# Performance work log

Hardware: AMD Instinct MI355X
Metric: run time of the kernel (lower is better)

Reference implementation:

```python
import jax, jax.numpy as jnp
import numpy as np


def _gru(x, Wih, Whh, bih, bhh):
    """Single-layer torch-style GRU, batch_first. x:[B,T,E], Wih:[3H,E], Whh:[3H,H]."""
    gi = jnp.einsum('bte,ge->btg', x, Wih) + bih  # precompute input gates [B,T,3H]
    H = Whh.shape[1]
    h0 = jnp.zeros((x.shape[0], H), x.dtype)

    def step(h, gi_t):
        gh = h @ Whh.T + bhh
        i_r, i_z, i_n = jnp.split(gi_t, 3, axis=-1)
        h_r, h_z, h_n = jnp.split(gh, 3, axis=-1)
        r = jax.nn.sigmoid(i_r + h_r)
        z = jax.nn.sigmoid(i_z + h_z)
        n = jnp.tanh(i_n + r * h_n)
        h_new = (1.0 - z) * n + z * h
        return h_new, h_new

    _, hs = jax.lax.scan(step, h0, jnp.swapaxes(gi, 0, 1))
    return jnp.swapaxes(hs, 0, 1)  # [B,T,H]


def setup_inputs() -> dict:
    V, E, H, B, S, Tc, Ts = 100000, 256, 256, 256, 10, 20, 50
    Bc = B * S
    k = jax.random.split(jax.random.key(0), 16)
    w = lambda kk, shp, s=0.05: (jax.random.normal(kk, shp) * s).astype(jnp.float32)
    return {
        'input_cate_batch': jax.random.randint(k[0], (Bc, Tc), 0, V),
        'mask_cate_batch': jnp.ones((Bc, Tc), jnp.float32),
        'mask_cate_seq_batch': jnp.ones((B, S), jnp.float32),
        'max_actionNum_cate_batch': Tc,
        'max_subseqNum_cate_batch': S,
        'subseqLen_cate_batch': jax.random.randint(k[1], (Bc,), 0, Tc),
        'seqLen_cate_batch': jax.random.randint(k[2], (B,), 0, S),
        'input_batch': jax.random.randint(k[3], (B, Ts), 0, V),
        'mask_batch': jnp.ones((B, Ts), jnp.float32),
        'seqLen_batch': jax.random.randint(k[4], (B,), 0, Ts),
        'target_y_batch': jax.random.randint(k[5], (B,), 0, V),
        'train_test_flag': 0,
        'emb': w(k[6], (V, E), 0.02),
        'Wih_c': w(k[7], (3 * H, E)), 'Whh_c': w(k[8], (3 * H, H)),
        'bih_c': jnp.zeros((3 * H,), jnp.float32), 'bhh_c': jnp.zeros((3 * H,), jnp.float32),
        'Wih_s': w(k[9], (3 * H, E)), 'Whh_s': w(k[10], (3 * H, H)),
        'bih_s': jnp.zeros((3 * H,), jnp.float32), 'bhh_s': jnp.zeros((3 * H,), jnp.float32),
        'fc_W': w(k[11], (H, 2 * H)), 'fc_b': jnp.zeros((H,), jnp.float32),
    }


def reference(input_cate_batch, mask_cate_batch, mask_cate_seq_batch,
              max_actionNum_cate_batch, max_subseqNum_cate_batch,
              subseqLen_cate_batch, seqLen_cate_batch, input_batch, mask_batch,
              seqLen_batch, target_y_batch, train_test_flag,
              emb, Wih_c, Whh_c, bih_c, bhh_c, Wih_s, Whh_s, bih_s, bhh_s,
              fc_W, fc_b):
    Bc = input_cate_batch.shape[0]
    B = input_batch.shape[0]
    S = max_subseqNum_cate_batch
    # --- category GRU over subsequences ---
    x_c = emb[input_cate_batch]                                  # [Bc,Tc,E]
    out_c = _gru(x_c, Wih_c, Whh_c, bih_c, bhh_c) * mask_cate_batch[:, :, None]
    gathered = out_c[jnp.arange(Bc), subseqLen_cate_batch]       # [Bc,H] per-row length gather
    seq_cate = gathered.reshape(B, S, -1)                        # [B,S,H]
    # --- short GRU over the recent session ---
    x_s = emb[input_batch]                                       # [B,Ts,E]
    out_s = _gru(x_s, Wih_s, Whh_s, bih_s, bhh_s) * mask_batch[:, :, None]
    out_short = out_s[jnp.arange(B), seqLen_batch]               # [B,H]
    # --- masked softmax attention of short state over subseq states ---
    att = jnp.einsum('bsh,bh->bs', seq_cate, out_short)          # [B,S]
    w = jax.nn.softmax(att, axis=1) * mask_cate_seq_batch
    w = w / jnp.sum(w, axis=1, keepdims=True)
    sum_cate = jnp.einsum('bs,bsh->bh', w, seq_cate)             # [B,H]
    mix = jnp.concatenate([sum_cate, out_short], axis=1)         # [B,2H]
    fc_out = mix @ fc_W.T + fc_b                                 # [B,H]
    logits = fc_out @ emb.T                                      # [B,V] shared-embedding output layer
    return logits, target_y_batch
```

## Files before the change

### kernel.cpp

```cpp
#include <hip/hip_runtime.h>
#include <cmath>

#define EMB_V 100000
#define BATCH 256
#define SUBS  10
#define BC    2560
#define TC    20
#define TS    50

using bf16x8 = __attribute__((ext_vector_type(8))) short;
using f32x4  = __attribute__((ext_vector_type(4))) float;

__device__ __forceinline__ unsigned short f2bf(float f) {
    unsigned int u = __float_as_uint(f);
    u += 0x7fff + ((u >> 16) & 1);
    return (unsigned short)(u >> 16);
}
__device__ __forceinline__ float bf2f(unsigned short u) {
    return __uint_as_float(((unsigned int)u) << 16);
}
__device__ __forceinline__ float bf_lo(unsigned u) { return __uint_as_float(u << 16); }
__device__ __forceinline__ float bf_hi(unsigned u) { return __uint_as_float(u & 0xffff0000u); }
__device__ __forceinline__ float sigmoid_fast(float x) {
    return __builtin_amdgcn_rcpf(1.f + __expf(-x));
}
__device__ __forceinline__ float tanh_fast(float x) {
    float e = __expf(2.f * x);
    return 1.f - 2.f * __builtin_amdgcn_rcpf(e + 1.f);
}
__device__ __forceinline__ void dma16(const void* g, void* l) {
    __builtin_amdgcn_global_load_lds((const __attribute__((address_space(1))) void*)g,
                                     (__attribute__((address_space(3))) void*)l, 16, 0, 0);
}

__device__ __forceinline__ void pack_whh_dev(const float* __restrict__ W,
                                             unsigned short* __restrict__ P, int t) {
    if (t >= 48 * 8 * 64) return;
    int l = t & 63, kc = (t >> 6) & 7, nt = t >> 9;
    int g = nt % 3, cg = nt / 3;
    int n = g * 256 + (cg >> 1) * 32 + 2 * (l & 15) + (cg & 1);
    int k = kc * 32 + (l >> 4) * 8;
    const float* src = W + n * 256 + k;
    unsigned short* dst = P + (size_t)t * 8;
#pragma unroll
    for (int j = 0; j < 8; ++j) dst[j] = f2bf(src[j]);
}
__global__ __launch_bounds__(256) void prep_misc(
    const float* __restrict__ fc_W, float* __restrict__ fcWT,
    const float* __restrict__ Whh_c, unsigned short* __restrict__ packW_c,
    const float* __restrict__ Whh_s, unsigned short* __restrict__ packW_s,
    const float* __restrict__ Wih_c, unsigned short* __restrict__ wihb_c,
    const float* __restrict__ Wih_s, unsigned short* __restrict__ wihb_s)
{
    const int b = blockIdx.x, tid = threadIdx.x;
    if (b < 512) {
        int o = b * 256 + tid;
        int c = o >> 8, r = o & 255;
        fcWT[o] = fc_W[r * 512 + c];
    } else if (b < 608) {
        pack_whh_dev(Whh_c, packW_c, (b - 512) * 256 + tid);
    } else if (b < 704) {
        pack_whh_dev(Whh_s, packW_s, (b - 608) * 256 + tid);
    } else if (b < 896) {
        int i = (b - 704) * 256 + tid;
        float4 v = ((const float4*)Wih_c)[i];
        ((ushort4*)wihb_c)[i] = make_ushort4(f2bf(v.x), f2bf(v.y), f2bf(v.z), f2bf(v.w));
    } else {
        int i = (b - 896) * 256 + tid;
        float4 v = ((const float4*)Wih_s)[i];
        ((ushort4*)wihb_s)[i] = make_ushort4(f2bf(v.x), f2bf(v.y), f2bf(v.z), f2bf(v.w));
    }
}

__global__ void f32_to_bf16(const float* __restrict__ in, unsigned short* __restrict__ out,
                            int n4) {
    for (int i = blockIdx.x * 256 + threadIdx.x; i < n4; i += gridDim.x * 256) {
        float4 v = ((const float4*)in)[i];
        ((ushort4*)out)[i] = make_ushort4(f2bf(v.x), f2bf(v.y), f2bf(v.z), f2bf(v.w));
    }
}

template <bool GATHER, bool OBF16, bool NGUARD>
__global__ __launch_bounds__(256, 3) void gemm_abt(
    const unsigned short* __restrict__ A, const int* __restrict__ tok,
    const unsigned short* __restrict__ B, void* __restrict__ Cout,
    int N, int ldc)
{
    __shared__ unsigned short Asub[128 * 64];
    __shared__ unsigned short Bsub[128 * 64];
    const int tid = threadIdx.x;
    const int l = tid & 63, wave = tid >> 6;
    const int lm = l & 15, quad = l >> 4;
    const int wm = wave >> 1, wn = wave & 1;
    const int n0 = blockIdx.x * 128, m0 = blockIdx.y * 128;

    unsigned aofs[4], bofs[4];
#pragma unroll
    for (int i = 0; i < 4; ++i) {
        int c = tid + i * 256, row = c >> 3, cc = c & 7;
        int sw = cc ^ (row & 7);
        aofs[i] = (GATHER ? (unsigned)tok[m0 + row] : (unsigned)(m0 + row)) * 256u + sw * 8u;
        unsigned brow = (unsigned)(n0 + row);
        if (NGUARD && brow >= (unsigned)N) brow = (unsigned)N - 1;
        bofs[i] = brow * 256u + sw * 8u;
    }
    const int dstu = (tid & 192) * 8;
    const int fsw = lm & 7;

    f32x4 acc[4][4];
#pragma unroll
    for (int mi = 0; mi < 4; ++mi)
#pragma unroll
        for (int ni = 0; ni < 4; ++ni) acc[mi][ni] = (f32x4){0.f, 0.f, 0.f, 0.f};

    for (int kk = 0; kk < 4; ++kk) {
        const int k0 = kk * 64;
#pragma unroll
        for (int i = 0; i < 4; ++i)
            dma16(A + aofs[i] + k0, &Asub[dstu + i * 2048]);
#pragma unroll
        for (int i = 0; i < 4; ++i)
            dma16(B + bofs[i] + k0, &Bsub[dstu + i * 2048]);
        __syncthreads();
#pragma unroll
        for (int kc = 0; kc < 2; ++kc) {
            const int ch = ((kc * 4 + quad) ^ fsw) * 8;
            bf16x8 af[4], bfv[4];
#pragma unroll
            for (int mi = 0; mi < 4; ++mi)
                af[mi] = *(const bf16x8*)&Asub[(wm * 64 + mi * 16 + lm) * 64 + ch];
#pragma unroll
            for (int ni = 0; ni < 4; ++ni)
                bfv[ni] = *(const bf16x8*)&Bsub[(wn * 64 + ni * 16 + lm) * 64 + ch];
#pragma unroll
            for (int mi = 0; mi < 4; ++mi)
#pragma unroll
                for (int ni = 0; ni < 4; ++ni)
                    acc[mi][ni] = __builtin_amdgcn_mfma_f32_16x16x32_bf16(
                        af[mi], bfv[ni], acc[mi][ni], 0, 0, 0);
        }
        __syncthreads();
    }
#pragma unroll
    for (int mi = 0; mi < 4; ++mi)
#pragma unroll
        for (int ni = 0; ni < 4; ++ni) {
            int col = n0 + wn * 64 + ni * 16 + lm;
            if (NGUARD && col >= N) continue;
#pragma unroll
            for (int i = 0; i < 4; ++i) {
                int row = m0 + wm * 64 + mi * 16 + quad * 4 + i;
                if (OBF16)
                    ((unsigned short*)Cout)[(size_t)row * ldc + col] = f2bf(acc[mi][ni][i]);
                else
                    ((float*)Cout)[(size_t)row * ldc + col] = acc[mi][ni][i];
            }
        }
}

__global__ __launch_bounds__(512, 1) void gru_scan_fused(
    const unsigned short* __restrict__ gi_c, const unsigned short* __restrict__ pW_c,
    const float* __restrict__ bih_c, const float* __restrict__ bhh_c,
    const int* __restrict__ len_c, const float* __restrict__ mask_c,
    float* __restrict__ out_c,
    const unsigned short* __restrict__ gi_s, const unsigned short* __restrict__ pW_s,
    const float* __restrict__ bih_s, const float* __restrict__ bhh_s,
    const int* __restrict__ len_s, const float* __restrict__ mask_s,
    float* __restrict__ out_s)
{
    __shared__ unsigned short h_lds[2][16][264];
    __shared__ unsigned short b_lds[8 * 8 * 512];

    const bool is_cat = blockIdx.x < (BC / 16);
    const int  T      = is_cat ? TC : TS;
    const int  R      = is_cat ? blockIdx.x : blockIdx.x - BC / 16;
    const int  row0   = R * 16;
    const unsigned short* gi   = is_cat ? gi_c  : gi_s;
    const unsigned short* pW   = is_cat ? pW_c  : pW_s;
    const float*          bih  = is_cat ? bih_c : bih_s;
    const float*          bhh  = is_cat ? bhh_c : bhh_s;
    const int*            lenp = is_cat ? len_c : len_s;
    const float*          mask = is_cat ? mask_c : mask_s;
    float*                outp = is_cat ? out_c : out_s;

    const int tid  = threadIdx.x;
    const int l    = tid & 63, w = tid >> 6;
    const int lm   = l & 15,   quad = l >> 4;

    for (int i = tid; i < 2 * 16 * 264; i += 512) ((unsigned short*)h_lds)[i] = 0;

    bf16x8 breg[40];
#pragma unroll
    for (int ti = 0; ti < 6; ++ti)
#pragma unroll
        for (int kc = 0; kc < 8; ++kc) {
            bf16x8 v = *((const bf16x8*)pW + (size_t)((6 * w + ti) * 8 + kc) * 64 + l);
            if (ti < 5) breg[ti * 8 + kc] = v;
            else        *(bf16x8*)&b_lds[((w * 8 + kc) * 64 + l) * 8] = v;
        }

    const int c0p = 32 * w + 2 * lm;
    const float cR0 = bih[c0p] + bhh[c0p],             cR1 = bih[c0p + 1] + bhh[c0p + 1];
    const float cZ0 = bih[256 + c0p] + bhh[256 + c0p], cZ1 = bih[257 + c0p] + bhh[257 + c0p];
    const float cNi0 = bih[512 + c0p], cNi1 = bih[513 + c0p];
    const float cNh0 = bhh[512 + c0p], cNh1 = bhh[513 + c0p];

    int len[4];
    const unsigned short* gpa[4];
#pragma unroll
    for (int i = 0; i < 4; ++i) {
        const int r = quad * 4 + i;
        len[i] = lenp[row0 + r];
        gpa[i] = gi + (size_t)(row0 + r) * T * 768 + c0p;
    }

    float hold0[4] = {0.f, 0.f, 0.f, 0.f};
    float hold1[4] = {0.f, 0.f, 0.f, 0.f};

    __syncthreads();

    for (int t = 0; t < T; ++t) {
        unsigned gv[4][3];
#pragma unroll
        for (int i = 0; i < 4; ++i) {
            const unsigned short* p = gpa[i];
            gv[i][0] = *(const unsigned*)(p);
            gv[i][1] = *(const unsigned*)(p + 256);
            gv[i][2] = *(const unsigned*)(p + 512);
            gpa[i] = p + 768;
        }

        const unsigned short (*hb)[264] = h_lds[t & 1];
        f32x4 acc[6];
#pragma unroll
        for (int ti = 0; ti < 6; ++ti) acc[ti] = (f32x4){0.f, 0.f, 0.f, 0.f};
#pragma unroll
        for (int kc = 0; kc < 8; ++kc) {
            bf16x8 a = *(const bf16x8*)&hb[lm][kc * 32 + quad * 8];
#pragma unroll
            for (int ti = 0; ti < 6; ++ti) {
                bf16x8 b = (ti < 5) ? breg[ti * 8 + kc]
                                    : *(const bf16x8*)&b_lds[((w * 8 + kc) * 64 + l) * 8];
                acc[ti] = __builtin_amdgcn_mfma_f32_16x16x32_bf16(a, b, acc[ti], 0, 0, 0);
            }
        }

        unsigned short (*hw)[264] = h_lds[(t + 1) & 1];
#pragma unroll
        for (int i = 0; i < 4; ++i) {
            const int r = quad * 4 + i;
            float rg0 = sigmoid_fast(bf_lo(gv[i][0]) + acc[0][i] + cR0);
            float rg1 = sigmoid_fast(bf_hi(gv[i][0]) + acc[3][i] + cR1);
            float zg0 = sigmoid_fast(bf_lo(gv[i][1]) + acc[1][i] + cZ0);
            float zg1 = sigmoid_fast(bf_hi(gv[i][1]) + acc[4][i] + cZ1);
            float ng0 = tanh_fast(bf_lo(gv[i][2]) + cNi0 + rg0 * (acc[2][i] + cNh0));
            float ng1 = tanh_fast(bf_hi(gv[i][2]) + cNi1 + rg1 * (acc[5][i] + cNh1));
            float hn0 = zg0 * (hold0[i] - ng0) + ng0;
            float hn1 = zg1 * (hold1[i] - ng1) + ng1;
            hold0[i] = hn0; hold1[i] = hn1;
            *(unsigned*)&hw[r][c0p] = (unsigned)f2bf(hn0) | ((unsigned)f2bf(hn1) << 16);
            if (t == len[i]) {
                float m = mask[(row0 + r) * T + t];
                *(float2*)&outp[(size_t)(row0 + r) * 256 + c0p] = make_float2(hn0 * m, hn1 * m);
            }
        }

        asm volatile("s_waitcnt lgkmcnt(0)" ::: "memory");
        __builtin_amdgcn_sched_barrier(0);
        __builtin_amdgcn_s_barrier();
        __builtin_amdgcn_sched_barrier(0);
    }
}

__global__ __launch_bounds__(256) void attn_fc(
    const float* __restrict__ seq_cate, const float* __restrict__ out_short,
    const float* __restrict__ mask_seq, const float* __restrict__ fcWT,
    const float* __restrict__ fc_b, const int* __restrict__ target,
    unsigned short* __restrict__ fc_out, float* __restrict__ d_out)
{
    __shared__ float sc[SUBS][256];
    __shared__ float os[256];
    __shared__ float part[SUBS][256];
    __shared__ float mix[512];
    const int b = blockIdx.x, tid = threadIdx.x;

    os[tid] = out_short[b * 256 + tid];
    for (int s = 0; s < SUBS; ++s) sc[s][tid] = seq_cate[(size_t)(b * SUBS + s) * 256 + tid];
    __syncthreads();

    for (int s = 0; s < SUBS; ++s) part[s][tid] = sc[s][tid] * os[tid];
    __syncthreads();
    for (int off = 128; off >= 1; off >>= 1) {
        if (tid < off)
            for (int s = 0; s < SUBS; ++s) part[s][tid] += part[s][tid + off];
        __syncthreads();
    }

    float w[SUBS];
    float m = -1e30f;
    for (int s = 0; s < SUBS; ++s) m = fmaxf(m, part[s][0]);
    float sum = 0.f;
    for (int s = 0; s < SUBS; ++s) { w[s] = __expf(part[s][0] - m); sum += w[s]; }
    float tot = 0.f;
    for (int s = 0; s < SUBS; ++s) { w[s] = (w[s] / sum) * mask_seq[b * SUBS + s]; tot += w[s]; }
    float inv = 1.f / tot;

    float sumc = 0.f;
    for (int s = 0; s < SUBS; ++s) sumc += w[s] * inv * sc[s][tid];
    mix[tid] = sumc;
    mix[256 + tid] = os[tid];
    __syncthreads();

    float acc = fc_b[tid];
    for (int jj = 0; jj < 512; ++jj) acc = fmaf(mix[jj], fcWT[jj * 256 + tid], acc);
    fc_out[b * 256 + tid] = f2bf(acc);

    if (tid == 0) d_out[(size_t)BATCH * EMB_V + b] = (float)target[b];
}

extern "C" void kernel_launch(void* const* d_in, const int* in_sizes, int n_in,
                              void* d_out, int out_size, void* d_ws, size_t ws_size,
                              hipStream_t stream) {
    const int*   input_cate   = (const int*)d_in[0];
    const float* mask_cate    = (const float*)d_in[1];
    const float* mask_seq     = (const float*)d_in[2];
    const int*   subseqLen    = (const int*)d_in[5];
    const int*   input_batch  = (const int*)d_in[7];
    const float* mask_batch   = (const float*)d_in[8];
    const int*   seqLen_batch = (const int*)d_in[9];
    const int*   target       = (const int*)d_in[10];
    const float* emb          = (const float*)d_in[12];
    const float* Wih_c        = (const float*)d_in[13];
    const float* Whh_c        = (const float*)d_in[14];
    const float* bih_c        = (const float*)d_in[15];
    const float* bhh_c        = (const float*)d_in[16];
    const float* Wih_s        = (const float*)d_in[17];
    const float* Whh_s        = (const float*)d_in[18];
    const float* bih_s        = (const float*)d_in[19];
    const float* bhh_s        = (const float*)d_in[20];
    const float* fc_W         = (const float*)d_in[21];
    const float* fc_b         = (const float*)d_in[22];
    float* out = (float*)d_out;

    float* ws = (float*)d_ws;
    float*          fcWT      = ws;
    float*          out_short = ws + 131072;
    unsigned short* fc_outb   = (unsigned short*)(ws + 196608);
    float*          seq_cate  = ws + 229376;
    unsigned short* packW_c   = (unsigned short*)(ws + 884736);
    unsigned short* packW_s   = (unsigned short*)(ws + 983040);
    unsigned short* wihb_c    = (unsigned short*)(ws + 1081344);
    unsigned short* wihb_s    = (unsigned short*)(ws + 1179648);
    unsigned short* embb      = (unsigned short*)(ws + 1277952);
    unsigned short* gi_c      = (unsigned short*)(ws + 14077952);
    unsigned short* gi_s      = (unsigned short*)(ws + 33738752);

    prep_misc<<<1088, 256, 0, stream>>>(fc_W, fcWT, Whh_c, packW_c, Whh_s, packW_s,
                                        Wih_c, wihb_c, Wih_s, wihb_s);
    f32_to_bf16<<<2048, 256, 0, stream>>>(emb, embb, EMB_V * 256 / 4);

    gemm_abt<true, true, false><<<dim3(6, 400), 256, 0, stream>>>(
        embb, input_cate, wihb_c, gi_c, 768, 768);
    gemm_abt<true, true, false><<<dim3(6, 100), 256, 0, stream>>>(
        embb, input_batch, wihb_s, gi_s, 768, 768);

    gru_scan_fused<<<BC / 16 + BATCH / 16, 512, 0, stream>>>(
        gi_c, packW_c, bih_c, bhh_c, subseqLen, mask_cate, seq_cate,
        gi_s, packW_s, bih_s, bhh_s, seqLen_batch, mask_batch, out_short);

    attn_fc<<<BATCH, 256, 0, stream>>>(
        seq_cate, out_short, mask_seq, fcWT, fc_b, target, fc_outb, out);

    gemm_abt<false, false, true><<<dim3(782, 2), 256, 0, stream>>>(
        fc_outb, nullptr, embb, out, EMB_V, EMB_V);
}
```

Before: 433.5 us.

## Trim GRU scan to max length, prefetch gates, keep weights in registers, swap grid

The GRU scan now stops at the largest length in each 16-row block plus one instead of running every timestep. This is valid because only the hidden state at step len is ever written out. The input-gate loads for the next step are double-buffered so they overlap the current step's MFMA work. All six weight tiles stay in registers, which removes the LDS copy of the sixth, at the cost of more register pressure. The output-logits GEMM swaps its grid axes so the two M-tiles that share each embedding tile run next to each other, which should improve L2 reuse.

```diff
diff --git a/kernel.cpp b/kernel.cpp
--- a/kernel.cpp
+++ b/kernel.cpp
@@ -80,7 +80,7 @@
     }
 }
 
-template <bool GATHER, bool OBF16, bool NGUARD>
+template <bool GATHER, bool OBF16, bool NGUARD, bool SWAPXY>
 __global__ __launch_bounds__(256, 3) void gemm_abt(
     const unsigned short* __restrict__ A, const int* __restrict__ tok,
     const unsigned short* __restrict__ B, void* __restrict__ Cout,
@@ -92,7 +92,9 @@
     const int l = tid & 63, wave = tid >> 6;
     const int lm = l & 15, quad = l >> 4;
     const int wm = wave >> 1, wn = wave & 1;
-    const int n0 = blockIdx.x * 128, m0 = blockIdx.y * 128;
+    const int bx = SWAPXY ? blockIdx.y : blockIdx.x;
+    const int by = SWAPXY ? blockIdx.x : blockIdx.y;
+    const int n0 = bx * 128, m0 = by * 128;
 
     unsigned aofs[4], bofs[4];
 #pragma unroll
@@ -169,7 +171,6 @@
     float* __restrict__ out_s)
 {
     __shared__ unsigned short h_lds[2][16][264];
-    __shared__ unsigned short b_lds[8 * 8 * 512];
 
     const bool is_cat = blockIdx.x < (BC / 16);
     const int  T      = is_cat ? TC : TS;
@@ -189,15 +190,12 @@
 
     for (int i = tid; i < 2 * 16 * 264; i += 512) ((unsigned short*)h_lds)[i] = 0;
 
-    bf16x8 breg[40];
+    bf16x8 breg[48];
 #pragma unroll
     for (int ti = 0; ti < 6; ++ti)
 #pragma unroll
-        for (int kc = 0; kc < 8; ++kc) {
-            bf16x8 v = *((const bf16x8*)pW + (size_t)((6 * w + ti) * 8 + kc) * 64 + l);
-            if (ti < 5) breg[ti * 8 + kc] = v;
-            else        *(bf16x8*)&b_lds[((w * 8 + kc) * 64 + l) * 8] = v;
-        }
+        for (int kc = 0; kc < 8; ++kc)
+            breg[ti * 8 + kc] = *((const bf16x8*)pW + (size_t)((6 * w + ti) * 8 + kc) * 64 + l);
 
     const int c0p = 32 * w + 2 * lm;
     const float cR0 = bih[c0p] + bhh[c0p],             cR1 = bih[c0p + 1] + bhh[c0p + 1];
@@ -205,6 +203,11 @@
     const float cNi0 = bih[512 + c0p], cNi1 = bih[513 + c0p];
     const float cNh0 = bhh[512 + c0p], cNh1 = bhh[513 + c0p];
 
+    int maxlen = 0;
+#pragma unroll
+    for (int k = 0; k < 16; ++k) maxlen = max(maxlen, lenp[row0 + k]);
+    const int Tend = maxlen + 1;
+
     int len[4];
     const unsigned short* gpa[4];
 #pragma unroll
@@ -217,10 +220,8 @@
     float hold0[4] = {0.f, 0.f, 0.f, 0.f};
     float hold1[4] = {0.f, 0.f, 0.f, 0.f};
 
-    __syncthreads();
-
-    for (int t = 0; t < T; ++t) {
-        unsigned gv[4][3];
+    unsigned ga[4][3], gb[4][3];
+    auto loadgi = [&](unsigned (&gv)[4][3]) {
 #pragma unroll
         for (int i = 0; i < 4; ++i) {
             const unsigned short* p = gpa[i];
@@ -229,7 +230,9 @@
             gv[i][2] = *(const unsigned*)(p + 512);
             gpa[i] = p + 768;
         }
-
+    };
+
+    auto stepf = [&](const unsigned (&gv)[4][3], int t) {
         const unsigned short (*hb)[264] = h_lds[t & 1];
         f32x4 acc[6];
 #pragma unroll
@@ -238,11 +241,8 @@
         for (int kc = 0; kc < 8; ++kc) {
             bf16x8 a = *(const bf16x8*)&hb[lm][kc * 32 + quad * 8];
 #pragma unroll
-            for (int ti = 0; ti < 6; ++ti) {
-                bf16x8 b = (ti < 5) ? breg[ti * 8 + kc]
-                                    : *(const bf16x8*)&b_lds[((w * 8 + kc) * 64 + l) * 8];
-                acc[ti] = __builtin_amdgcn_mfma_f32_16x16x32_bf16(a, b, acc[ti], 0, 0, 0);
-            }
+            for (int ti = 0; ti < 6; ++ti)
+                acc[ti] = __builtin_amdgcn_mfma_f32_16x16x32_bf16(a, breg[ti * 8 + kc], acc[ti], 0, 0, 0);
         }
 
         unsigned short (*hw)[264] = h_lds[(t + 1) & 1];
@@ -269,6 +269,19 @@
         __builtin_amdgcn_sched_barrier(0);
         __builtin_amdgcn_s_barrier();
         __builtin_amdgcn_sched_barrier(0);
+    };
+
+    loadgi(ga);
+    __syncthreads();
+
+    int t = 0;
+    for (;;) {
+        if (t + 1 < Tend) loadgi(gb);
+        stepf(ga, t);
+        if (++t >= Tend) break;
+        if (t + 1 < Tend) loadgi(ga);
+        stepf(gb, t);
+        if (++t >= Tend) break;
     }
 }
 
@@ -359,9 +372,9 @@
                                         Wih_c, wihb_c, Wih_s, wihb_s);
     f32_to_bf16<<<2048, 256, 0, stream>>>(emb, embb, EMB_V * 256 / 4);
 
-    gemm_abt<true, true, false><<<dim3(6, 400), 256, 0, stream>>>(
+    gemm_abt<true, true, false, false><<<dim3(6, 400), 256, 0, stream>>>(
         embb, input_cate, wihb_c, gi_c, 768, 768);
-    gemm_abt<true, true, false><<<dim3(6, 100), 256, 0, stream>>>(
+    gemm_abt<true, true, false, false><<<dim3(6, 100), 256, 0, stream>>>(
         embb, input_batch, wihb_s, gi_s, 768, 768);
 
     gru_scan_fused<<<BC / 16 + BATCH / 16, 512, 0, stream>>>(
@@ -371,6 +384,6 @@
     attn_fc<<<BATCH, 256, 0, stream>>>(
         seq_cate, out_short, mask_seq, fcWT, fc_b, target, fc_outb, out);
 
-    gemm_abt<false, false, true><<<dim3(782, 2), 256, 0, stream>>>(
+    gemm_abt<false, false, true, true><<<dim3(2, 782), 256, 0, stream>>>(
         fc_outb, nullptr, embb, out, EMB_V, EMB_V);
 }
```

Result: slower. 506.7 us (+16.9%).
